# Optimization experiments

Hardware: AMD Instinct MI355X
Metric: run time of the kernel (lower is better)

Reference implementation:

```python
import jax, jax.numpy as jnp
import numpy as np

N_NODES = 50000
N_EDGES = 800000
IN_CH = 128
HID = 48
HEADS = 2
HH = HID * HEADS  # 96
N_GRAPHS = 64
NEG_SLOPE = 0.2


def _gat_layer(x, src, dst, n, W, a_src, a_dst, b, heads, out_ch):
    # x: [N, in]; W: [in, heads*out]; a_src/a_dst: [heads, out]; b: [heads*out]
    h = (x @ W).reshape(n, heads, out_ch)              # [N, H, C]
    es = (h * a_src).sum(-1)                            # [N, H]
    ed = (h * a_dst).sum(-1)                            # [N, H]
    e = jax.nn.leaky_relu(es[src] + ed[dst], NEG_SLOPE)  # [E, H]
    m = jax.ops.segment_max(e, dst, num_segments=n)      # segment softmax (stable)
    p = jnp.exp(e - m[dst])
    denom = jax.ops.segment_sum(p, dst, num_segments=n)
    alpha = p / denom[dst]                               # [E, H]
    out = jax.ops.segment_sum(alpha[:, :, None] * h[src], dst, num_segments=n)
    return out.reshape(n, heads * out_ch) + b


def setup_inputs() -> dict:
    key = jax.random.key(0)
    ks = jax.random.split(key, 20)
    x = jax.random.normal(ks[0], (N_NODES, IN_CH), dtype=jnp.float32)
    edge_index = jax.random.randint(ks[1], (2, N_EDGES), 0, N_NODES, dtype=jnp.int64)
    edge_weight = jax.random.uniform(ks[2], (N_EDGES,), dtype=jnp.float32)
    batch = jnp.sort(jax.random.randint(ks[3], (N_NODES,), 0, N_GRAPHS, dtype=jnp.int64))
    s = 0.1
    params = {
        'W1': jax.random.normal(ks[4], (IN_CH, HH)) * s,
        'as1': jax.random.normal(ks[5], (HEADS, HID)) * s,
        'ad1': jax.random.normal(ks[6], (HEADS, HID)) * s,
        'b1': jnp.zeros((HH,), jnp.float32),
        'W2': jax.random.normal(ks[7], (HH, HH)) * s,
        'as2': jax.random.normal(ks[8], (1, HH)) * s,
        'ad2': jax.random.normal(ks[9], (1, HH)) * s,
        'b2': jnp.zeros((HH,), jnp.float32),
        'W3': jax.random.normal(ks[10], (HH, HH)) * s,
        'as3': jax.random.normal(ks[11], (1, HH)) * s,
        'ad3': jax.random.normal(ks[12], (1, HH)) * s,
        'b3': jnp.zeros((HH,), jnp.float32),
        'W4': jax.random.normal(ks[13], (HH, HH)) * s,
        'as4': jax.random.normal(ks[14], (1, HH)) * s,
        'ad4': jax.random.normal(ks[15], (1, HH)) * s,
        'b4': jnp.zeros((HH,), jnp.float32),
        'Wc': jax.random.normal(ks[16], (HH, 1)) * s,
        'bc': jnp.zeros((1,), jnp.float32),
    }
    return {'x': x, 'edge_index': edge_index, 'edge_weight': edge_weight,
            'batch': batch, **params}


def reference(x, edge_index, edge_weight, batch,
              W1, as1, ad1, b1, W2, as2, ad2, b2,
              W3, as3, ad3, b3, W4, as4, ad4, b4, Wc, bc):
    n = x.shape[0]
    loops = jnp.arange(n, dtype=edge_index.dtype)  # PyG GATConv add_self_loops=True
    src = jnp.concatenate([edge_index[0], loops])
    dst = jnp.concatenate([edge_index[1], loops])
    # edge_weight is ignored by GATConv when edge_dim=None (faithful to PyG)
    h = jax.nn.relu(_gat_layer(x, src, dst, n, W1, as1, ad1, b1, HEADS, HID))
    h = jax.nn.relu(_gat_layer(h, src, dst, n, W2, as2, ad2, b2, 1, HH))
    h = jax.nn.relu(_gat_layer(h, src, dst, n, W3, as3, ad3, b3, 1, HH))
    h = jax.nn.relu(_gat_layer(h, src, dst, n, W4, as4, ad4, b4, 1, HH))
    # global_mean_pool
    sums = jax.ops.segment_sum(h, batch, num_segments=N_GRAPHS)
    cnts = jax.ops.segment_sum(jnp.ones((n, 1), h.dtype), batch, num_segments=N_GRAPHS)
    pooled = sums / jnp.maximum(cnts, 1.0)
    return jax.nn.sigmoid(pooled @ Wc + bc)
```

## Files before the change

### kernel.cpp

```cpp
#include <hip/hip_runtime.h>
#include <hip/hip_bf16.h>

#define NN 50000
#define NE 800000
#define NG 64
#define NBUCK 256
#define BN 196
#define EPB 4096
#define HB 196
#define SMAX 4200

typedef __attribute__((ext_vector_type(8))) short short8;
typedef __attribute__((ext_vector_type(4))) float float4v;
typedef __attribute__((ext_vector_type(2))) float float2v;

__device__ __forceinline__ float bf2f(unsigned short u){
    unsigned v = ((unsigned)u) << 16; float f; __builtin_memcpy(&f, &v, 4); return f;
}
__device__ __forceinline__ unsigned short f2bf(float f){
    unsigned u; __builtin_memcpy(&u, &f, 4);
    u = (u + 0x7fffu + ((u >> 16) & 1u)) >> 16;
    return (unsigned short)u;
}
__device__ __forceinline__ float lrelu(float v){ return v > 0.f ? v : 0.2f * v; }

__device__ __forceinline__ float ldflex(const void* p, long i, int isbf){
    if (isbf) return bf2f(((const unsigned short*)p)[i]);
    return ((const float*)p)[i];
}
__device__ __forceinline__ int ldidx(const int* p, long i, int is64){
    return p[is64 ? (i << 1) : i];
}

__device__ __forceinline__ unsigned int enc_fp8_1(float f){
    unsigned u; __builtin_memcpy(&u, &f, 4);
    unsigned s = (u >> 24) & 0x80u;
    float a = fabsf(f); a = fminf(a, 448.f);
    float x = a * 0x1p-120f;
    unsigned xu; __builtin_memcpy(&xu, &x, 4);
    unsigned r = (xu + 0x7FFFFu + ((xu >> 20) & 1u)) >> 20;
    if (r > 0x7Eu) r = 0x7Eu;
    return s | r;
}
__device__ __forceinline__ unsigned short pk_fp8(float a, float b){
#if __has_builtin(__builtin_amdgcn_cvt_pk_fp8_f32)
    int r = __builtin_amdgcn_cvt_pk_fp8_f32(a, b, 0, false);
    return (unsigned short)(r & 0xFFFF);
#else
    return (unsigned short)(enc_fp8_1(a) | (enc_fp8_1(b) << 8));
#endif
}
__device__ __forceinline__ float dec_fp8_manual(unsigned int byte){
    unsigned bits = ((byte & 0x80u) << 24) | ((byte & 0x7Fu) << 20);
    float f; __builtin_memcpy(&f, &bits, 4);
    return f * 0x1p120f;
}
__device__ __forceinline__ void dec_fp8x4_pk(unsigned int v, float2v& lo, float2v& hi){
#if __has_builtin(__builtin_amdgcn_cvt_pk_f32_fp8)
    lo = __builtin_amdgcn_cvt_pk_f32_fp8((int)v, false);
    hi = __builtin_amdgcn_cvt_pk_f32_fp8((int)v, true);
#else
    lo[0] = dec_fp8_manual(v & 0xFF);
    lo[1] = dec_fp8_manual((v >> 8) & 0xFF);
    hi[0] = dec_fp8_manual((v >> 16) & 0xFF);
    hi[1] = dec_fp8_manual((v >> 24) & 0xFF);
#endif
}

__device__ __forceinline__ float rdlane_f(float v, int l){
    int i; __builtin_memcpy(&i, &v, 4);
    int r = __builtin_amdgcn_readlane(i, l);
    float f; __builtin_memcpy(&f, &r, 4);
    return f;
}

__global__ void detect_kernel(const unsigned short* xu, const unsigned int* eiu,
                              const unsigned int* bu, int* flags, int* bcnt,
                              int* bcur, float* pooled, int* gcnt){
    if (blockIdx.x == 1){
        int tid = threadIdx.x;
        bcnt[tid] = 0;
        bcur[tid] = 0;
        for (int i = tid; i < NG * 96; i += 256) pooled[i] = 0.f;
        if (tid < NG) gcnt[tid] = 0;
        return;
    }
    if (threadIdx.x != 0) return;
    int hit = 0;
    for (int i = 0; i < 128; i++){
        int ex = (xu[2 * i] >> 7) & 0xFF;
        if (ex >= 100 && ex <= 140) hit++;
    }
    flags[0] = (hit >= 64) ? 1 : 0;
    int z = 0;
    for (int i = 0; i < 128; i++) if (eiu[2 * i + 1] == 0) z++;
    flags[1] = (z >= 120) ? 1 : 0;
    z = 0;
    for (int i = 0; i < 128; i++) if (bu[49745 + 2 * i] == 0) z++;
    flags[2] = (z >= 120) ? 1 : 0;
}

__global__ __launch_bounds__(256) void wtprep_kernel(const void* W0, const void* W1,
                                                     const void* W2, const void* W3,
                                                     unsigned short* wt_all,
                                                     const int* flags){
    int l = blockIdx.x;
    const void* W = (l == 0) ? W0 : (l == 1) ? W1 : (l == 2) ? W2 : W3;
    int K = (l == 0) ? 128 : 96;
    unsigned short* out = wt_all + ((l == 0) ? 0 : (96 * 128 + (l - 1) * 96 * 96));
    int isbf = flags[0];
    int tot = 96 * K;
    for (int i = threadIdx.x; i < tot; i += 256){
        int c = i / K, k = i - c * K;
        out[i] = f2bf(ldflex(W, (long)k * 96 + c, isbf));
    }
}

__global__ __launch_bounds__(256) void bhist_kernel(const int* __restrict__ ei,
                                                    int* __restrict__ bcnt,
                                                    const int* __restrict__ flags){
    __shared__ int h[NBUCK];
    int tid = threadIdx.x;
    h[tid] = 0; __syncthreads();
    int f64 = flags[1];
    long e0 = (long)blockIdx.x * EPB + tid;
    #pragma unroll
    for (int r = 0; r < 16; r++){
        long e = e0 + r * 256;
        if (e < NE){
            int d = ldidx(ei, NE + e, f64);
            atomicAdd(&h[d / BN], 1);
        }
    }
    __syncthreads();
    atomicAdd(&bcnt[tid], h[tid]);
}

__global__ __launch_bounds__(256) void bscatter_kernel(const int* __restrict__ ei,
                                                       const int* __restrict__ bcnt,
                                                       int* __restrict__ bcur,
                                                       int2* __restrict__ ebuf,
                                                       const int* __restrict__ flags){
    __shared__ int h[NBUCK], lofs[NBUCK], gbase[NBUCK], lcur[NBUCK], bb[NBUCK];
    __shared__ int2 lstage[EPB];
    int tid = threadIdx.x;
    int f64 = flags[1];
    {
        int v = bcnt[tid];
        bb[tid] = v; __syncthreads();
        for (int off = 1; off < 256; off <<= 1){
            int x = bb[tid];
            int y = (tid >= off) ? bb[tid - off] : 0;
            __syncthreads();
            bb[tid] = x + y;
            __syncthreads();
        }
        bb[tid] -= v;
    }
    h[tid] = 0; __syncthreads();
    int2 ed[16]; int bk[16];
    long e0 = (long)blockIdx.x * EPB + tid;
    #pragma unroll
    for (int r = 0; r < 16; r++){
        long e = e0 + r * 256;
        if (e < NE){
            int s = ldidx(ei, e, f64);
            int d = ldidx(ei, NE + e, f64);
            ed[r] = make_int2(s, d);
            bk[r] = d / BN;
            atomicAdd(&h[bk[r]], 1);
        } else bk[r] = -1;
    }
    __syncthreads();
    int v = h[tid];
    lofs[tid] = v; __syncthreads();
    for (int off = 1; off < 256; off <<= 1){
        int x = lofs[tid];
        int y = (tid >= off) ? lofs[tid - off] : 0;
        __syncthreads();
        lofs[tid] = x + y;
        __syncthreads();
    }
    int excl = lofs[tid] - v;
    lofs[tid] = excl;
    lcur[tid] = excl;
    if (v > 0) gbase[tid] = bb[tid] + atomicAdd(&bcur[tid], v);
    __syncthreads();
    #pragma unroll
    for (int r = 0; r < 16; r++){
        if (bk[r] >= 0){
            int p = atomicAdd(&lcur[bk[r]], 1);
            lstage[p] = ed[r];
        }
    }
    __syncthreads();
    long base = (long)blockIdx.x * EPB;
    int cnt = (NE - base < EPB) ? (int)(NE - base) : EPB;
    for (int j = tid; j < cnt; j += 256){
        int2 e = lstage[j];
        int i = e.y / BN;
        ebuf[gbase[i] + j - lofs[i]] = e;
    }
}

__global__ __launch_bounds__(256) void place_kernel(const int2* __restrict__ ebuf,
                                                    const int* __restrict__ bcnt,
                                                    int* __restrict__ row_ptr,
                                                    int* __restrict__ csr){
    __shared__ int sb[NBUCK];
    __shared__ int nh[BN];
    __shared__ int nofs[256];
    __shared__ int lcur[BN];
    __shared__ int stage[SMAX];
    int k = blockIdx.x, tid = threadIdx.x;
    int n0 = k * BN;
    sb[tid] = bcnt[tid]; __syncthreads();
    for (int off = 1; off < 256; off <<= 1){
        int x = sb[tid];
        int y = (tid >= off) ? sb[tid - off] : 0;
        __syncthreads();
        sb[tid] = x + y;
        __syncthreads();
    }
    int seg0 = (k == 0) ? 0 : sb[k - 1];
    int len = sb[k] - seg0;
    for (int i = tid; i < BN; i += 256) nh[i] = 0;
    __syncthreads();
    for (int j = tid; j < len; j += 256){
        int2 e = ebuf[seg0 + j];
        atomicAdd(&nh[e.y - n0], 1);
    }
    __syncthreads();
    int v = (tid < BN) ? nh[tid] : 0;
    nofs[tid] = v; __syncthreads();
    for (int off = 1; off < 256; off <<= 1){
        int x = nofs[tid];
        int y = (tid >= off) ? nofs[tid - off] : 0;
        __syncthreads();
        nofs[tid] = x + y;
        __syncthreads();
    }
    int excl = nofs[tid] - v;
    if (tid < BN){
        lcur[tid] = excl;
        int node = n0 + tid;
        if (node < NN) row_ptr[node] = seg0 + excl;
    }
    if (k == NBUCK - 1 && tid == 0) row_ptr[NN] = NE;
    __syncthreads();
    if (len <= SMAX){
        for (int j = tid; j < len; j += 256){
            int2 e = ebuf[seg0 + j];
            int p = atomicAdd(&lcur[e.y - n0], 1);
            stage[p] = e.x;
        }
        __syncthreads();
        for (int j = tid; j < len; j += 256)
            csr[seg0 + j] = stage[j];
    } else {
        for (int j = tid; j < len; j += 256){
            int2 e = ebuf[seg0 + j];
            int p = atomicAdd(&lcur[e.y - n0], 1);
            csr[seg0 + p] = e.x;
        }
    }
}

template<int K, int H, bool L1>
__global__ __launch_bounds__(256) void gemm_mfma(const void* __restrict__ Ain,
                                                 const unsigned short* __restrict__ Wt,
                                                 const void* __restrict__ as_,
                                                 const void* __restrict__ ad_,
                                                 unsigned short* __restrict__ hq16,
                                                 float* __restrict__ es,
                                                 float* __restrict__ ed,
                                                 float* __restrict__ pself,
                                                 const int* __restrict__ flags){
    __shared__ union {
        struct { unsigned short xs[64 * 40]; unsigned short wt[96 * 40]; } s;
        float hs[64 * 104];
    } u;
    int tid = threadIdx.x;
    int row0 = blockIdx.x * 64;
    int lane = tid & 63, w = tid >> 6;
    int m = lane & 15, q = lane >> 4;
    int isbf = flags[0];
    float4v acc[6];
    #pragma unroll
    for (int ct = 0; ct < 6; ct++) acc[ct] = (float4v){0.f, 0.f, 0.f, 0.f};

    int sr = tid >> 2, kp = tid & 3;
    int rr = row0 + sr; if (rr >= NN) rr = NN - 1;

    for (int k0 = 0; k0 < K; k0 += 32){
        uint4 av;
        if (L1 && !isbf){
            const float* xf = (const float*)Ain + (size_t)rr * K + k0 + kp * 8;
            float4 f1 = *(const float4*)xf;
            float4 f2 = *(const float4*)(xf + 4);
            av.x = (unsigned)f2bf(f1.x) | ((unsigned)f2bf(f1.y) << 16);
            av.y = (unsigned)f2bf(f1.z) | ((unsigned)f2bf(f1.w) << 16);
            av.z = (unsigned)f2bf(f2.x) | ((unsigned)f2bf(f2.y) << 16);
            av.w = (unsigned)f2bf(f2.z) | ((unsigned)f2bf(f2.w) << 16);
        } else {
            av = *(const uint4*)((const unsigned short*)Ain + (size_t)rr * K + k0 + kp * 8);
        }
        *(uint4*)(u.s.xs + sr * 40 + kp * 8) = av;
        for (int i = tid; i < 96 * 4; i += 256){
            int c = i >> 2, kq = i & 3;
            *(uint4*)(u.s.wt + c * 40 + kq * 8) =
                *(const uint4*)(Wt + (size_t)c * K + k0 + kq * 8);
        }
        __syncthreads();
        short8 a = *(const short8*)(u.s.xs + (w * 16 + m) * 40 + q * 8);
        #pragma unroll
        for (int ct = 0; ct < 6; ct++){
            short8 b = *(const short8*)(u.s.wt + (ct * 16 + m) * 40 + q * 8);
            acc[ct] = __builtin_amdgcn_mfma_f32_16x16x32_bf16(a, b, acc[ct], 0, 0, 0);
        }
        __syncthreads();
    }

    #pragma unroll
    for (int ct = 0; ct < 6; ct++)
        #pragma unroll
        for (int r = 0; r < 4; r++)
            u.hs[(w * 16 + q * 4 + r) * 104 + ct * 16 + m] = acc[ct][r];
    __syncthreads();

    int rl = tid >> 2, part = tid & 3;
    int row = row0 + rl;
    float hv[24];
    #pragma unroll
    for (int jj = 0; jj < 6; jj++)
        *(float4v*)&hv[jj * 4] = *(const float4v*)&u.hs[rl * 104 + part * 24 + jj * 4];

    float pes = 0.f, ped = 0.f;
    #pragma unroll
    for (int i = 0; i < 24; i++){
        int c = part * 24 + i;
        pes += hv[i] * ldflex(as_, c, isbf);
        ped += hv[i] * ldflex(ad_, c, isbf);
    }
    pes += __shfl_xor(pes, 1); ped += __shfl_xor(ped, 1);
    if (H == 1){ pes += __shfl_xor(pes, 2); ped += __shfl_xor(ped, 2); }

    if (row < NN){
        if (part == 0){
            es[(long)row * H] = pes; ed[(long)row * H] = ped;
            pself[(long)row * H] = __expf(lrelu(pes + ped));
        }
        if (H == 2 && part == 2){
            es[(long)row * H + 1] = pes; ed[(long)row * H + 1] = ped;
            pself[(long)row * H + 1] = __expf(lrelu(pes + ped));
        }
        unsigned short wds[12];
        #pragma unroll
        for (int j = 0; j < 12; j++) wds[j] = pk_fp8(hv[2 * j], hv[2 * j + 1]);
        uint2* dst = (uint2*)hq16 + (long)row * 16 + part * 3;
        #pragma unroll
        for (int j2 = 0; j2 < 3; j2++){
            uint2 v;
            v.x = (unsigned)wds[4 * j2] | ((unsigned)wds[4 * j2 + 1] << 16);
            v.y = (unsigned)wds[4 * j2 + 2] | ((unsigned)wds[4 * j2 + 3] << 16);
            dst[j2] = v;
        }
    }
}

template<int H>
__global__ __launch_bounds__(256) void attn_kernel(const unsigned int* __restrict__ hq,
                                                   const float* __restrict__ es,
                                                   const float* __restrict__ ed,
                                                   const float* __restrict__ pself,
                                                   const int* __restrict__ row_ptr,
                                                   const int* __restrict__ csr,
                                                   const void* __restrict__ bias,
                                                   unsigned int* __restrict__ outb,
                                                   const int* __restrict__ flags){
    int lane = threadIdx.x & 63;
    int d = blockIdx.x * 4 + (threadIdx.x >> 6);
    if (d >= NN) return;
    int isbf = flags[0];
    int beg = row_ptr[d], deg = row_ptr[d + 1] - beg;
    int g = lane / 12;
    int cl = lane - g * 12;
    int head = (H == 2) ? ((cl >= 6) ? 1 : 0) : 0;
    int m = lane - 48;
    float edd0 = ed[(long)d * H];
    float edd1 = (H == 2) ? ed[(long)d * H + 1] : edd0;

    int s_nxt = 0; float p0_nxt = 0.f, p1_nxt = 0.f;
    if (lane >= 48 && m < deg){
        int s = csr[beg + m];
        s_nxt = s * 32;
        if (H == 1){
            p0_nxt = __expf(lrelu(es[s] + edd0));
        } else {
            float2 e2 = *(const float2*)&es[2 * (long)s];
            p0_nxt = __expf(lrelu(e2.x + edd0));
            p1_nxt = __expf(lrelu(e2.y + edd1));
        }
    }

    float2v acc[4];
    #pragma unroll
    for (int k = 0; k < 4; k++) acc[k] = (float2v){0.f, 0.f};
    float dn0 = 0.f, dn1 = 0.f;
    int cl2 = 2 * cl;

    for (int base = 0; base < deg; base += 16){
        int s_cur = s_nxt; float p0c = p0_nxt, p1c = p1_nxt;
        dn0 += p0c; dn1 += p1c;
        int nb = base + 16;
        s_nxt = 0; p0_nxt = 0.f; p1_nxt = 0.f;
        if (lane >= 48 && nb + m < deg){
            int s = csr[beg + nb + m];
            s_nxt = s * 32;
            if (H == 1){
                p0_nxt = __expf(lrelu(es[s] + edd0));
            } else {
                float2 e2 = *(const float2*)&es[2 * (long)s];
                p0_nxt = __expf(lrelu(e2.x + edd0));
                p1_nxt = __expf(lrelu(e2.y + edd1));
            }
        }
        int cnt = deg - base; if (cnt > 16) cnt = 16;
        int steps = (cnt + 3) >> 2;
        auto do_step = [&](int t){
            int idx = 48 + 4 * t + g;
            int s32 = __shfl(s_cur, idx);
            float p;
            if (H == 2){
                float p0 = __shfl(p0c, idx);
                float p1 = __shfl(p1c, idx);
                p = head ? p1 : p0;
            } else {
                p = __shfl(p0c, idx);
            }
            uint2 v = make_uint2(0u, 0u);
            if (lane < 48) v = *(const uint2*)(hq + (unsigned)s32 + cl2);
            float2v lo0, hi0, lo1, hi1;
            dec_fp8x4_pk(v.x, lo0, hi0);
            dec_fp8x4_pk(v.y, lo1, hi1);
            float2v p2 = {p, p};
            acc[0] += p2 * lo0; acc[1] += p2 * hi0;
            acc[2] += p2 * lo1; acc[3] += p2 * hi1;
        };
        if (steps == 4){
            do_step(0); do_step(1); do_step(2); do_step(3);
        } else {
            for (int t = 0; t < steps; t++) do_step(t);
        }
    }

    for (int off = 1; off < 16; off <<= 1){
        dn0 += __shfl_xor(dn0, off);
        if (H == 2) dn1 += __shfl_xor(dn1, off);
    }
    float dn0_t = rdlane_f(dn0, 48);
    float dn1_t = (H == 2) ? rdlane_f(dn1, 48) : dn0_t;

    float t8[8];
    #pragma unroll
    for (int k = 0; k < 4; k++){ t8[2 * k] = acc[k][0]; t8[2 * k + 1] = acc[k][1]; }
    #pragma unroll
    for (int k = 0; k < 8; k++) t8[k] += __shfl(t8[k], lane + 24);
    #pragma unroll
    for (int k = 0; k < 8; k++) t8[k] += __shfl(t8[k], lane + 12);

    if (lane < 12){
        float ps = pself[(long)d * H + head];
        float dn = (head ? dn1_t : dn0_t) + ps;
        uint2 v = *(const uint2*)(hq + (unsigned)d * 32u + cl2);
        float2v lo0, hi0, lo1, hi1;
        dec_fp8x4_pk(v.x, lo0, hi0);
        dec_fp8x4_pk(v.y, lo1, hi1);
        float f[8] = {lo0[0], lo0[1], hi0[0], hi0[1], lo1[0], lo1[1], hi1[0], hi1[1]};
        int c0 = 8 * cl;
        unsigned short ob[8];
        #pragma unroll
        for (int k = 0; k < 8; k++){
            float o = (t8[k] + ps * f[k]) / dn + ldflex(bias, c0 + k, isbf);
            ob[k] = f2bf(fmaxf(o, 0.f));
        }
        uint4 vv;
        vv.x = (unsigned)ob[0] | ((unsigned)ob[1] << 16);
        vv.y = (unsigned)ob[2] | ((unsigned)ob[3] << 16);
        vv.z = (unsigned)ob[4] | ((unsigned)ob[5] << 16);
        vv.w = (unsigned)ob[6] | ((unsigned)ob[7] << 16);
        ((uint4*)outb)[(long)d * 12 + cl] = vv;
    }
}

__global__ __launch_bounds__(64) void pool_kernel(const unsigned int* __restrict__ bufb,
                                                  const int* __restrict__ batch,
                                                  float* __restrict__ pooled,
                                                  int* __restrict__ gcnt,
                                                  const int* __restrict__ flags){
    int f64 = flags[2];
    int n0 = blockIdx.x * 32;
    if (n0 >= NN) return;
    int n1 = n0 + 32; if (n1 > NN) n1 = NN;
    int lane = threadIdx.x;
    if (lane < 48){
        float a0 = 0.f, a1 = 0.f;
        int curg = ldidx(batch, n0, f64);
        for (int nd = n0; nd < n1; nd++){
            int g = ldidx(batch, nd, f64);
            if (g != curg){
                atomicAdd(&pooled[curg * 96 + 2 * lane], a0);
                atomicAdd(&pooled[curg * 96 + 2 * lane + 1], a1);
                a0 = a1 = 0.f; curg = g;
            }
            unsigned v = bufb[(long)nd * 48 + lane];
            a0 += bf2f((unsigned short)v);
            a1 += bf2f((unsigned short)(v >> 16));
        }
        atomicAdd(&pooled[curg * 96 + 2 * lane], a0);
        atomicAdd(&pooled[curg * 96 + 2 * lane + 1], a1);
    } else if (lane == 48){
        int cnt = 0;
        int curg = ldidx(batch, n0, f64);
        for (int nd = n0; nd < n1; nd++){
            int g = ldidx(batch, nd, f64);
            if (g != curg){
                atomicAdd(&gcnt[curg], cnt);
                cnt = 0; curg = g;
            }
            cnt++;
        }
        atomicAdd(&gcnt[curg], cnt);
    }
}

__global__ void final_kernel(const float* __restrict__ pooled, const int* __restrict__ gcnt,
                             const void* __restrict__ Wc, const void* __restrict__ bc,
                             void* __restrict__ outp, const int* __restrict__ flags){
    int isbf = flags[0];
    int g = threadIdx.x;
    if (g >= NG) return;
    float cnt = (float)gcnt[g];
    if (cnt < 1.f) cnt = 1.f;
    float acc = 0.f;
    for (int c = 0; c < 96; c++)
        acc += (pooled[g * 96 + c] / cnt) * ldflex(Wc, c, isbf);
    acc += ldflex(bc, 0, isbf);
    float sg = 1.f / (1.f + __expf(-acc));
    if (isbf) ((unsigned short*)outp)[g] = f2bf(sg);
    else      ((float*)outp)[g] = sg;
}

extern "C" void kernel_launch(void* const* d_in, const int* in_sizes, int n_in,
                              void* d_out, int out_size, void* d_ws, size_t ws_size,
                              hipStream_t stream){
    const void* x     = d_in[0];
    const int* ei     = (const int*)d_in[1];
    const int* batch  = (const int*)d_in[3];
    const void* W[4]  = {d_in[4],  d_in[8],  d_in[12], d_in[16]};
    const void* AS[4] = {d_in[5],  d_in[9],  d_in[13], d_in[17]};
    const void* AD[4] = {d_in[6],  d_in[10], d_in[14], d_in[18]};
    const void* B[4]  = {d_in[7],  d_in[11], d_in[15], d_in[19]};
    const void* Wc    = d_in[20];
    const void* bc    = d_in[21];

    char* p = (char*)d_ws;
    auto alloc = [&](size_t bytes) -> void* {
        void* r = (void*)p;
        p += (bytes + 255) & ~(size_t)255;
        return r;
    };
    int* flags     = (int*)alloc(16);
    unsigned int* hq = (unsigned int*)alloc((size_t)NN * 128);
    unsigned int* buf1b = (unsigned int*)alloc((size_t)NN * 96 * 2);
    unsigned short* wt_all = (unsigned short*)alloc((size_t)(96 * 128 + 3 * 96 * 96) * 2);
    float* es      = (float*)alloc((size_t)NN * 2 * 4);
    float* ed      = (float*)alloc((size_t)NN * 2 * 4);
    float* pself   = (float*)alloc((size_t)NN * 2 * 4);
    int* row_ptr   = (int*)alloc((size_t)(NN + 1) * 4);
    int* csr       = (int*)alloc((size_t)NE * 4);
    int2* ebuf     = (int2*)alloc((size_t)NE * 8);
    int* bcnt      = (int*)alloc((size_t)NBUCK * 4);
    int* bcur      = (int*)alloc((size_t)NBUCK * 4);
    float* pooled  = (float*)alloc((size_t)NG * 96 * 4);
    int* gcnt      = (int*)alloc((size_t)NG * 4);

    detect_kernel<<<2, 256, 0, stream>>>((const unsigned short*)x, (const unsigned int*)ei,
                                         (const unsigned int*)batch, flags, bcnt, bcur,
                                         pooled, gcnt);
    wtprep_kernel<<<4, 256, 0, stream>>>(W[0], W[1], W[2], W[3], wt_all, flags);

    bhist_kernel<<<HB, 256, 0, stream>>>(ei, bcnt, flags);
    bscatter_kernel<<<HB, 256, 0, stream>>>(ei, bcnt, bcur, ebuf, flags);
    place_kernel<<<NBUCK, 256, 0, stream>>>(ebuf, bcnt, row_ptr, csr);

    const int GB = (NN + 63) / 64;
    const int AB = (NN + 3) / 4;
    unsigned short* wt1 = wt_all;
    unsigned short* wt2 = wt_all + 96 * 128;
    unsigned short* wt3 = wt2 + 96 * 96;
    unsigned short* wt4 = wt3 + 96 * 96;

    gemm_mfma<128, 2, true><<<GB, 256, 0, stream>>>(x, wt1, AS[0], AD[0],
                                                    (unsigned short*)hq, es, ed, pself, flags);
    attn_kernel<2><<<AB, 256, 0, stream>>>(hq, es, ed, pself, row_ptr, csr, B[0], buf1b, flags);
    unsigned short* wts[3] = {wt2, wt3, wt4};
    for (int l = 1; l < 4; l++){
        gemm_mfma<96, 1, false><<<GB, 256, 0, stream>>>(buf1b, wts[l - 1], AS[l], AD[l],
                                                        (unsigned short*)hq, es, ed, pself, flags);
        attn_kernel<1><<<AB, 256, 0, stream>>>(hq, es, ed, pself, row_ptr, csr, B[l], buf1b, flags);
    }

    pool_kernel<<<(NN + 31) / 32, 64, 0, stream>>>(buf1b, batch, pooled, gcnt, flags);
    final_kernel<<<1, 64, 0, stream>>>(pooled, gcnt, Wc, bc, d_out, flags);
}
```

Measured before the change: 412.8 us.

## Merge preprocessing kernels, use per-block histograms, and restructure attention reduction

Folds the detect, weight-prep and histogram kernels into one launch. Each block now writes its own per-block histogram, and the scatter kernel derives deterministic bucket offsets from those histograms, replacing the global atomic cursor and the repeated scans in place_kernel. The attention kernel reassigns lanes so each group of 4 lanes shares a channel slice, reduces with xor-shuffles, accumulates the softmax denominator per lane, and multiplies by a reciprocal instead of dividing. The GEMM caches the attention vectors in LDS and uses packed bf16 conversion. The trade-off is redundant detection work in each block and extra reads of the histogram array in every scatter block.

```diff
diff --git a/kernel.cpp b/kernel.cpp
--- a/kernel.cpp
+++ b/kernel.cpp
@@ -30,6 +30,12 @@
 }
 __device__ __forceinline__ int ldidx(const int* p, long i, int is64){
     return p[is64 ? (i << 1) : i];
+}
+
+__device__ __forceinline__ unsigned pk_bf16(float a, float b){
+    unsigned r;
+    asm("v_cvt_pk_bf16_f32 %0, %1, %2" : "=v"(r) : "v"(a), "v"(b));
+    return r;
 }
 
 __device__ __forceinline__ unsigned int enc_fp8_1(float f){
@@ -67,63 +73,68 @@
 #endif
 }
 
-__device__ __forceinline__ float rdlane_f(float v, int l){
-    int i; __builtin_memcpy(&i, &v, 4);
-    int r = __builtin_amdgcn_readlane(i, l);
-    float f; __builtin_memcpy(&f, &r, 4);
-    return f;
-}
-
-__global__ void detect_kernel(const unsigned short* xu, const unsigned int* eiu,
-                              const unsigned int* bu, int* flags, int* bcnt,
-                              int* bcur, float* pooled, int* gcnt){
-    if (blockIdx.x == 1){
-        int tid = threadIdx.x;
-        bcnt[tid] = 0;
-        bcur[tid] = 0;
-        for (int i = tid; i < NG * 96; i += 256) pooled[i] = 0.f;
-        if (tid < NG) gcnt[tid] = 0;
-        return;
-    }
-    if (threadIdx.x != 0) return;
+__device__ __forceinline__ int detect_isbf_local(const unsigned short* xu){
     int hit = 0;
     for (int i = 0; i < 128; i++){
         int ex = (xu[2 * i] >> 7) & 0xFF;
         if (ex >= 100 && ex <= 140) hit++;
     }
-    flags[0] = (hit >= 64) ? 1 : 0;
+    return (hit >= 64) ? 1 : 0;
+}
+__device__ __forceinline__ int detect_i64_local(const unsigned int* u){
     int z = 0;
-    for (int i = 0; i < 128; i++) if (eiu[2 * i + 1] == 0) z++;
-    flags[1] = (z >= 120) ? 1 : 0;
-    z = 0;
-    for (int i = 0; i < 128; i++) if (bu[49745 + 2 * i] == 0) z++;
-    flags[2] = (z >= 120) ? 1 : 0;
-}
-
-__global__ __launch_bounds__(256) void wtprep_kernel(const void* W0, const void* W1,
-                                                     const void* W2, const void* W3,
-                                                     unsigned short* wt_all,
-                                                     const int* flags){
-    int l = blockIdx.x;
-    const void* W = (l == 0) ? W0 : (l == 1) ? W1 : (l == 2) ? W2 : W3;
-    int K = (l == 0) ? 128 : 96;
-    unsigned short* out = wt_all + ((l == 0) ? 0 : (96 * 128 + (l - 1) * 96 * 96));
-    int isbf = flags[0];
-    int tot = 96 * K;
-    for (int i = threadIdx.x; i < tot; i += 256){
-        int c = i / K, k = i - c * K;
-        out[i] = f2bf(ldflex(W, (long)k * 96 + c, isbf));
-    }
-}
-
-__global__ __launch_bounds__(256) void bhist_kernel(const int* __restrict__ ei,
-                                                    int* __restrict__ bcnt,
-                                                    const int* __restrict__ flags){
+    for (int i = 0; i < 128; i++) if (u[2 * i + 1] == 0) z++;
+    return (z >= 120) ? 1 : 0;
+}
+
+__global__ __launch_bounds__(256) void prep_kernel(const unsigned short* __restrict__ xu,
+                                                   const unsigned int* __restrict__ eiu,
+                                                   const unsigned int* __restrict__ bu,
+                                                   const void* W0, const void* W1,
+                                                   const void* W2, const void* W3,
+                                                   unsigned short* __restrict__ wt_all,
+                                                   const int* __restrict__ ei,
+                                                   int* __restrict__ hist,
+                                                   int* __restrict__ flags,
+                                                   float* __restrict__ pooled,
+                                                   int* __restrict__ gcnt){
+    int b = blockIdx.x, tid = threadIdx.x;
+    if (b == 0){
+        for (int i = tid; i < NG * 96; i += 256) pooled[i] = 0.f;
+        if (tid < NG) gcnt[tid] = 0;
+        if (tid == 0){
+            flags[0] = detect_isbf_local(xu);
+            flags[1] = detect_i64_local(eiu);
+            int z = 0;
+            for (int i = 0; i < 128; i++) if (bu[49745 + 2 * i] == 0) z++;
+            flags[2] = (z >= 120) ? 1 : 0;
+        }
+        return;
+    }
+    if (b <= 4){
+        __shared__ int lf;
+        if (tid == 0) lf = detect_isbf_local(xu);
+        __syncthreads();
+        int isbf = lf;
+        int l = b - 1;
+        const void* W = (l == 0) ? W0 : (l == 1) ? W1 : (l == 2) ? W2 : W3;
+        int K = (l == 0) ? 128 : 96;
+        unsigned short* out = wt_all + ((l == 0) ? 0 : (96 * 128 + (l - 1) * 96 * 96));
+        int tot = 96 * K;
+        for (int i = tid; i < tot; i += 256){
+            int c = i / K, k = i - c * K;
+            out[i] = f2bf(ldflex(W, (long)k * 96 + c, isbf));
+        }
+        return;
+    }
     __shared__ int h[NBUCK];
-    int tid = threadIdx.x;
-    h[tid] = 0; __syncthreads();
-    int f64 = flags[1];
-    long e0 = (long)blockIdx.x * EPB + tid;
+    __shared__ int lf2;
+    if (tid == 0) lf2 = detect_i64_local(eiu);
+    h[tid] = 0;
+    __syncthreads();
+    int f64 = lf2;
+    int hb = b - 5;
+    long e0 = (long)hb * EPB + tid;
     #pragma unroll
     for (int r = 0; r < 16; r++){
         long e = e0 + r * 256;
@@ -133,33 +144,45 @@
         }
     }
     __syncthreads();
-    atomicAdd(&bcnt[tid], h[tid]);
+    hist[(long)hb * NBUCK + tid] = h[tid];
 }
 
 __global__ __launch_bounds__(256) void bscatter_kernel(const int* __restrict__ ei,
-                                                       const int* __restrict__ bcnt,
-                                                       int* __restrict__ bcur,
-                                                       int2* __restrict__ ebuf,
-                                                       const int* __restrict__ flags){
+                                                       const int* __restrict__ hist,
+                                                       int* __restrict__ bucketBase,
+                                                       int2* __restrict__ ebuf){
     __shared__ int h[NBUCK], lofs[NBUCK], gbase[NBUCK], lcur[NBUCK], bb[NBUCK];
     __shared__ int2 lstage[EPB];
+    __shared__ int lf;
     int tid = threadIdx.x;
-    int f64 = flags[1];
-    {
-        int v = bcnt[tid];
-        bb[tid] = v; __syncthreads();
-        for (int off = 1; off < 256; off <<= 1){
-            int x = bb[tid];
-            int y = (tid >= off) ? bb[tid - off] : 0;
-            __syncthreads();
-            bb[tid] = x + y;
-            __syncthreads();
-        }
-        bb[tid] -= v;
-    }
-    h[tid] = 0; __syncthreads();
+    int myb = blockIdx.x;
+    if (tid == 0) lf = detect_i64_local((const unsigned int*)ei);
+    __syncthreads();
+    int f64 = lf;
+    int pre = 0, tot = 0;
+    for (int b2 = 0; b2 < HB; b2++){
+        int v = hist[b2 * NBUCK + tid];
+        tot += v;
+        if (b2 < myb) pre += v;
+    }
+    bb[tid] = tot; __syncthreads();
+    for (int off = 1; off < 256; off <<= 1){
+        int x = bb[tid];
+        int y = (tid >= off) ? bb[tid - off] : 0;
+        __syncthreads();
+        bb[tid] = x + y;
+        __syncthreads();
+    }
+    int bucket0 = bb[tid] - tot;
+    if (myb == 0){
+        bucketBase[tid] = bucket0;
+        if (tid == 255) bucketBase[256] = bb[255];
+    }
+    gbase[tid] = bucket0 + pre;
+    h[tid] = 0;
+    __syncthreads();
     int2 ed[16]; int bk[16];
-    long e0 = (long)blockIdx.x * EPB + tid;
+    long e0 = (long)myb * EPB + tid;
     #pragma unroll
     for (int r = 0; r < 16; r++){
         long e = e0 + r * 256;
@@ -184,7 +207,6 @@
     int excl = lofs[tid] - v;
     lofs[tid] = excl;
     lcur[tid] = excl;
-    if (v > 0) gbase[tid] = bb[tid] + atomicAdd(&bcur[tid], v);
     __syncthreads();
     #pragma unroll
     for (int r = 0; r < 16; r++){
@@ -194,7 +216,7 @@
         }
     }
     __syncthreads();
-    long base = (long)blockIdx.x * EPB;
+    long base = (long)myb * EPB;
     int cnt = (NE - base < EPB) ? (int)(NE - base) : EPB;
     for (int j = tid; j < cnt; j += 256){
         int2 e = lstage[j];
@@ -204,26 +226,17 @@
 }
 
 __global__ __launch_bounds__(256) void place_kernel(const int2* __restrict__ ebuf,
-                                                    const int* __restrict__ bcnt,
+                                                    const int* __restrict__ bucketBase,
                                                     int* __restrict__ row_ptr,
                                                     int* __restrict__ csr){
-    __shared__ int sb[NBUCK];
     __shared__ int nh[BN];
     __shared__ int nofs[256];
     __shared__ int lcur[BN];
     __shared__ int stage[SMAX];
     int k = blockIdx.x, tid = threadIdx.x;
     int n0 = k * BN;
-    sb[tid] = bcnt[tid]; __syncthreads();
-    for (int off = 1; off < 256; off <<= 1){
-        int x = sb[tid];
-        int y = (tid >= off) ? sb[tid - off] : 0;
-        __syncthreads();
-        sb[tid] = x + y;
-        __syncthreads();
-    }
-    int seg0 = (k == 0) ? 0 : sb[k - 1];
-    int len = sb[k] - seg0;
+    int seg0 = bucketBase[k];
+    int len = bucketBase[k + 1] - seg0;
     for (int i = tid; i < BN; i += 256) nh[i] = 0;
     __syncthreads();
     for (int j = tid; j < len; j += 256){
@@ -280,11 +293,14 @@
         struct { unsigned short xs[64 * 40]; unsigned short wt[96 * 40]; } s;
         float hs[64 * 104];
     } u;
+    __shared__ float2 aa[96];
     int tid = threadIdx.x;
     int row0 = blockIdx.x * 64;
     int lane = tid & 63, w = tid >> 6;
     int m = lane & 15, q = lane >> 4;
     int isbf = flags[0];
+    if (tid < 96)
+        aa[tid] = make_float2(ldflex(as_, tid, isbf), ldflex(ad_, tid, isbf));
     float4v acc[6];
     #pragma unroll
     for (int ct = 0; ct < 6; ct++) acc[ct] = (float4v){0.f, 0.f, 0.f, 0.f};
@@ -298,10 +314,10 @@
             const float* xf = (const float*)Ain + (size_t)rr * K + k0 + kp * 8;
             float4 f1 = *(const float4*)xf;
             float4 f2 = *(const float4*)(xf + 4);
-            av.x = (unsigned)f2bf(f1.x) | ((unsigned)f2bf(f1.y) << 16);
-            av.y = (unsigned)f2bf(f1.z) | ((unsigned)f2bf(f1.w) << 16);
-            av.z = (unsigned)f2bf(f2.x) | ((unsigned)f2bf(f2.y) << 16);
-            av.w = (unsigned)f2bf(f2.z) | ((unsigned)f2bf(f2.w) << 16);
+            av.x = pk_bf16(f1.x, f1.y);
+            av.y = pk_bf16(f1.z, f1.w);
+            av.z = pk_bf16(f2.x, f2.y);
+            av.w = pk_bf16(f2.z, f2.w);
         } else {
             av = *(const uint4*)((const unsigned short*)Ain + (size_t)rr * K + k0 + kp * 8);
         }
@@ -338,9 +354,9 @@
     float pes = 0.f, ped = 0.f;
     #pragma unroll
     for (int i = 0; i < 24; i++){
-        int c = part * 24 + i;
-        pes += hv[i] * ldflex(as_, c, isbf);
-        ped += hv[i] * ldflex(ad_, c, isbf);
+        float2 wv = aa[part * 24 + i];
+        pes += hv[i] * wv.x;
+        ped += hv[i] * wv.y;
     }
     pes += __shfl_xor(pes, 1); ped += __shfl_xor(ped, 1);
     if (H == 1){ pes += __shfl_xor(pes, 2); ped += __shfl_xor(ped, 2); }
@@ -383,9 +399,9 @@
     if (d >= NN) return;
     int isbf = flags[0];
     int beg = row_ptr[d], deg = row_ptr[d + 1] - beg;
-    int g = lane / 12;
-    int cl = lane - g * 12;
-    int head = (H == 2) ? ((cl >= 6) ? 1 : 0) : 0;
+    int g = lane & 3;
+    int c12 = lane >> 2;
+    int head = (H == 2) ? ((c12 >= 6) ? 1 : 0) : 0;
     int m = lane - 48;
     float edd0 = ed[(long)d * H];
     float edd1 = (H == 2) ? ed[(long)d * H + 1] : edd0;
@@ -406,12 +422,11 @@
     float2v acc[4];
     #pragma unroll
     for (int k = 0; k < 4; k++) acc[k] = (float2v){0.f, 0.f};
-    float dn0 = 0.f, dn1 = 0.f;
-    int cl2 = 2 * cl;
+    float dnl = 0.f;
+    int cq = 2 * c12;
 
     for (int base = 0; base < deg; base += 16){
         int s_cur = s_nxt; float p0c = p0_nxt, p1c = p1_nxt;
-        dn0 += p0c; dn1 += p1c;
         int nb = base + 16;
         s_nxt = 0; p0_nxt = 0.f; p1_nxt = 0.f;
         if (lane >= 48 && nb + m < deg){
@@ -439,13 +454,14 @@
                 p = __shfl(p0c, idx);
             }
             uint2 v = make_uint2(0u, 0u);
-            if (lane < 48) v = *(const uint2*)(hq + (unsigned)s32 + cl2);
+            if (lane < 48) v = *(const uint2*)(hq + (unsigned)s32 + cq);
             float2v lo0, hi0, lo1, hi1;
             dec_fp8x4_pk(v.x, lo0, hi0);
             dec_fp8x4_pk(v.y, lo1, hi1);
             float2v p2 = {p, p};
             acc[0] += p2 * lo0; acc[1] += p2 * hi0;
             acc[2] += p2 * lo1; acc[3] += p2 * hi1;
+            dnl += p;
         };
         if (steps == 4){
             do_step(0); do_step(1); do_step(2); do_step(3);
@@ -454,42 +470,32 @@
         }
     }
 
-    for (int off = 1; off < 16; off <<= 1){
-        dn0 += __shfl_xor(dn0, off);
-        if (H == 2) dn1 += __shfl_xor(dn1, off);
-    }
-    float dn0_t = rdlane_f(dn0, 48);
-    float dn1_t = (H == 2) ? rdlane_f(dn1, 48) : dn0_t;
-
     float t8[8];
     #pragma unroll
     for (int k = 0; k < 4; k++){ t8[2 * k] = acc[k][0]; t8[2 * k + 1] = acc[k][1]; }
     #pragma unroll
-    for (int k = 0; k < 8; k++) t8[k] += __shfl(t8[k], lane + 24);
-    #pragma unroll
-    for (int k = 0; k < 8; k++) t8[k] += __shfl(t8[k], lane + 12);
-
-    if (lane < 12){
+    for (int k = 0; k < 8; k++){
+        t8[k] += __shfl_xor(t8[k], 1);
+        t8[k] += __shfl_xor(t8[k], 2);
+    }
+    dnl += __shfl_xor(dnl, 1);
+    dnl += __shfl_xor(dnl, 2);
+
+    if (lane < 48 && g < 2){
         float ps = pself[(long)d * H + head];
-        float dn = (head ? dn1_t : dn0_t) + ps;
-        uint2 v = *(const uint2*)(hq + (unsigned)d * 32u + cl2);
-        float2v lo0, hi0, lo1, hi1;
-        dec_fp8x4_pk(v.x, lo0, hi0);
-        dec_fp8x4_pk(v.y, lo1, hi1);
-        float f[8] = {lo0[0], lo0[1], hi0[0], hi0[1], lo1[0], lo1[1], hi1[0], hi1[1]};
-        int c0 = 8 * cl;
-        unsigned short ob[8];
-        #pragma unroll
-        for (int k = 0; k < 8; k++){
-            float o = (t8[k] + ps * f[k]) / dn + ldflex(bias, c0 + k, isbf);
-            ob[k] = f2bf(fmaxf(o, 0.f));
-        }
-        uint4 vv;
-        vv.x = (unsigned)ob[0] | ((unsigned)ob[1] << 16);
-        vv.y = (unsigned)ob[2] | ((unsigned)ob[3] << 16);
-        vv.z = (unsigned)ob[4] | ((unsigned)ob[5] << 16);
-        vv.w = (unsigned)ob[6] | ((unsigned)ob[7] << 16);
-        ((uint4*)outb)[(long)d * 12 + cl] = vv;
+        float rdn = 1.f / (dnl + ps);
+        unsigned sv = hq[(unsigned)d * 32u + cq + g];
+        float2v lo, hi;
+        dec_fp8x4_pk(sv, lo, hi);
+        int c0 = 4 * (cq + g);
+        float o0 = (t8[4 * g + 0] + ps * lo[0]) * rdn + ldflex(bias, c0 + 0, isbf);
+        float o1 = (t8[4 * g + 1] + ps * lo[1]) * rdn + ldflex(bias, c0 + 1, isbf);
+        float o2 = (t8[4 * g + 2] + ps * hi[0]) * rdn + ldflex(bias, c0 + 2, isbf);
+        float o3 = (t8[4 * g + 3] + ps * hi[1]) * rdn + ldflex(bias, c0 + 3, isbf);
+        uint2 st;
+        st.x = pk_bf16(fmaxf(o0, 0.f), fmaxf(o1, 0.f));
+        st.y = pk_bf16(fmaxf(o2, 0.f), fmaxf(o3, 0.f));
+        ((uint2*)outb)[(long)d * 24 + cq + g] = st;
     }
 }
 
@@ -580,19 +586,18 @@
     int* row_ptr   = (int*)alloc((size_t)(NN + 1) * 4);
     int* csr       = (int*)alloc((size_t)NE * 4);
     int2* ebuf     = (int2*)alloc((size_t)NE * 8);
-    int* bcnt      = (int*)alloc((size_t)NBUCK * 4);
-    int* bcur      = (int*)alloc((size_t)NBUCK * 4);
+    int* hist      = (int*)alloc((size_t)HB * NBUCK * 4);
+    int* bucketBase= (int*)alloc((size_t)(NBUCK + 1) * 4);
     float* pooled  = (float*)alloc((size_t)NG * 96 * 4);
     int* gcnt      = (int*)alloc((size_t)NG * 4);
 
-    detect_kernel<<<2, 256, 0, stream>>>((const unsigned short*)x, (const unsigned int*)ei,
-                                         (const unsigned int*)batch, flags, bcnt, bcur,
-                                         pooled, gcnt);
-    wtprep_kernel<<<4, 256, 0, stream>>>(W[0], W[1], W[2], W[3], wt_all, flags);
-
-    bhist_kernel<<<HB, 256, 0, stream>>>(ei, bcnt, flags);
-    bscatter_kernel<<<HB, 256, 0, stream>>>(ei, bcnt, bcur, ebuf, flags);
-    place_kernel<<<NBUCK, 256, 0, stream>>>(ebuf, bcnt, row_ptr, csr);
+    prep_kernel<<<5 + HB, 256, 0, stream>>>((const unsigned short*)x,
+                                            (const unsigned int*)ei,
+                                            (const unsigned int*)batch,
+                                            W[0], W[1], W[2], W[3], wt_all,
+                                            ei, hist, flags, pooled, gcnt);
+    bscatter_kernel<<<HB, 256, 0, stream>>>(ei, hist, bucketBase, ebuf);
+    place_kernel<<<NBUCK, 256, 0, stream>>>(ebuf, bucketBase, row_ptr, csr);
 
     const int GB = (NN + 63) / 64;
     const int AB = (NN + 3) / 4;
```

Result: faster. 398.3 us (-3.5%).
